# Performance work log

Measured on AMD Instinct MI355X. Metric: run time of the kernel, lower is better.

## Reference

```python
import jax, jax.numpy as jnp
import numpy as np

N = 8192
IN_F = 512
OUT_F = 256


def mish(x):
    return x * jnp.tanh(jax.nn.softplus(x))


def setup_inputs() -> dict:
    key = jax.random.key(0)
    k1, k2, k3, k4 = jax.random.split(key, 4)
    inp = jax.random.normal(k1, (N, IN_F), dtype=jnp.float32)
    # random binary adjacency mask (float, used via adj > 0), ensure self-loops
    adj = jax.random.randint(k2, (N, N), 0, 2).astype(jnp.float32)
    adj = adj.at[jnp.arange(N), jnp.arange(N)].set(1.0)
    # xavier_uniform_ init
    lim_W = float(np.sqrt(6.0 / (IN_F + OUT_F)))
    W = jax.random.uniform(k3, (IN_F, OUT_F), minval=-lim_W, maxval=lim_W, dtype=jnp.float32)
    lim_a = float(np.sqrt(6.0 / (2 * OUT_F + 1)))
    a = jax.random.uniform(k4, (2 * OUT_F, 1), minval=-lim_a, maxval=lim_a, dtype=jnp.float32)
    return {"input": inp, "adj": adj, "W": W, "a": a}


def reference(input, adj, W, a):
    # h: [N, F_out]
    h = input @ W
    f_out = W.shape[1]
    a1 = a[:f_out, 0]   # applied to source node (row i)
    a2 = a[f_out:, 0]   # applied to target node (col j)
    # e[i, j] = mish(h_i . a1 + h_j . a2)  -- identical math to the
    # O(N^2*2F) concat([h_i, h_j]) @ a in the torch reference.
    e = mish((h @ a1)[:, None] + (h @ a2)[None, :])  # [N, N]
    attention = jnp.where(adj > 0, e, jnp.float32(-9e15))
    attention = jax.nn.softmax(attention, axis=1)
    # dropout is inference-off (training=False)
    h_prime = attention @ h  # [N, F_out]
    return mish(h_prime)
```

## Files before the change

### kernel.cpp

```cpp
#include <hip/hip_runtime.h>

typedef __attribute__((ext_vector_type(8))) short short8;
typedef __attribute__((ext_vector_type(4))) float f32x4;

#define L2E 1.44269504088896340736f

__device__ __forceinline__ unsigned short f2bf(float x) {
    union { float f; unsigned int u; } v; v.f = x;
    unsigned int u = v.u;
    unsigned int r = (u + 0x7FFFu + ((u >> 16) & 1u)) >> 16;
    return (unsigned short)r;
}

__device__ __forceinline__ float mishf(float x) {
    float u = __builtin_amdgcn_exp2f(x * L2E);
    float t = u * (u + 2.0f);
    return x * t * __builtin_amdgcn_rcpf(t + 2.0f);
}

__device__ __forceinline__ short pw(unsigned int mb, int j, float sv, float s1v) {
    float xL = s1v + sv;
    float u = __builtin_amdgcn_exp2f(xL);
    float t = u * (u + 2.0f);
    float m = xL * t * __builtin_amdgcn_rcpf(t + 2.0f);
    float p = __builtin_amdgcn_exp2f(m);
    union { float f; unsigned int u; } b; b.f = p;
    unsigned short h = (unsigned short)((b.u + 0x8000u) >> 16);
    return ((mb >> j) & 1u) ? (short)h : (short)0;
}

typedef __attribute__((address_space(1))) const unsigned int guint;
typedef __attribute__((address_space(3))) unsigned int luint;
__device__ __forceinline__ void lds16(const void* g, void* l) {
    __builtin_amdgcn_global_load_lds((guint*)g, (luint*)l, 16, 0, 0);
}

__global__ __launch_bounds__(256) void k_pack(const float* __restrict__ adj,
                                              unsigned int* __restrict__ mask) {
    int wid = blockIdx.x * 4 + (threadIdx.x >> 6);
    int lane = threadIdx.x & 63;
    const float* row = adj + (size_t)wid * 8192 + lane;
    unsigned int* mrow = mask + wid * 256;
#pragma unroll 2
    for (int base = 0; base < 8192; base += 256) {
        float v0 = row[base];
        float v1 = row[base + 64];
        float v2 = row[base + 128];
        float v3 = row[base + 192];
        unsigned long long b0 = __ballot(v0 > 0.5f);
        unsigned long long b1 = __ballot(v1 > 0.5f);
        unsigned long long b2 = __ballot(v2 > 0.5f);
        unsigned long long b3 = __ballot(v3 > 0.5f);
        if (lane == 0) {
            *(ulonglong2*)(mrow + (base >> 5))     = make_ulonglong2(b0, b1);
            *(ulonglong2*)(mrow + (base >> 5) + 4) = make_ulonglong2(b2, b3);
        }
    }
}

__global__ void k_cvt_wt(const float* __restrict__ W, unsigned short* __restrict__ wt) {
    int c = blockIdx.x;
    int t = threadIdx.x;
    wt[c * 512 + t]       = f2bf(W[(size_t)t * 256 + c]);
    wt[c * 512 + t + 256] = f2bf(W[(size_t)(t + 256) * 256 + c]);
}

__global__ __launch_bounds__(256) void k_gemm_h(const float* __restrict__ input,
                                                const unsigned short* __restrict__ wt,
                                                const float* __restrict__ a,
                                                unsigned short* __restrict__ hbt,
                                                float* __restrict__ s1L,
                                                float* __restrict__ s2L) {
    __shared__ float red[2][4][16];
    int tid = threadIdx.x;
    int w = tid >> 6, lane = tid & 63, g = lane >> 4, r = lane & 15;
    int base = blockIdx.x * 16;

    f32x4 acc[4];
#pragma unroll
    for (int n = 0; n < 4; ++n) acc[n] = (f32x4)0.0f;

    const float* arow = input + (size_t)(base + r) * 512 + g * 8;
    const unsigned short* wp = wt + (size_t)(w * 64 + r) * 512 + g * 8;
#pragma unroll 4
    for (int kb = 0; kb < 512; kb += 32) {
        float4 a0 = *(const float4*)(arow + kb);
        float4 a1 = *(const float4*)(arow + kb + 4);
        short8 af;
        af[0] = (short)f2bf(a0.x); af[1] = (short)f2bf(a0.y);
        af[2] = (short)f2bf(a0.z); af[3] = (short)f2bf(a0.w);
        af[4] = (short)f2bf(a1.x); af[5] = (short)f2bf(a1.y);
        af[6] = (short)f2bf(a1.z); af[7] = (short)f2bf(a1.w);
#pragma unroll
        for (int n2 = 0; n2 < 4; ++n2) {
            short8 bf = *(const short8*)(wp + n2 * 8192 + kb);
            acc[n2] = __builtin_amdgcn_mfma_f32_16x16x32_bf16(af, bf, acc[n2], 0, 0, 0);
        }
    }
    int rowc = base + g * 4;
#pragma unroll
    for (int n2 = 0; n2 < 4; ++n2) {
        int col = w * 64 + n2 * 16 + r;
        ushort4 pk;
        pk.x = f2bf(acc[n2][0]); pk.y = f2bf(acc[n2][1]);
        pk.z = f2bf(acc[n2][2]); pk.w = f2bf(acc[n2][3]);
        *(ushort4*)(hbt + (size_t)col * 8192 + rowc) = pk;
    }
    float p1[4] = {0,0,0,0}, p2[4] = {0,0,0,0};
#pragma unroll
    for (int n2 = 0; n2 < 4; ++n2) {
        float a1v = a[w * 64 + n2 * 16 + r];
        float a2v = a[256 + w * 64 + n2 * 16 + r];
#pragma unroll
        for (int i = 0; i < 4; ++i) {
            p1[i] += acc[n2][i] * a1v;
            p2[i] += acc[n2][i] * a2v;
        }
    }
#pragma unroll
    for (int off = 8; off >= 1; off >>= 1) {
#pragma unroll
        for (int i = 0; i < 4; ++i) {
            p1[i] += __shfl_xor(p1[i], off);
            p2[i] += __shfl_xor(p2[i], off);
        }
    }
    if (r == 0) {
#pragma unroll
        for (int i = 0; i < 4; ++i) {
            red[0][w][g * 4 + i] = p1[i];
            red[1][w][g * 4 + i] = p2[i];
        }
    }
    __syncthreads();
    if (tid < 16) {
        float s1 = red[0][0][tid] + red[0][1][tid] + red[0][2][tid] + red[0][3][tid];
        float s2 = red[1][0][tid] + red[1][1][tid] + red[1][2][tid] + red[1][3][tid];
        s1L[base + tid] = s1 * L2E;
        s2L[base + tid] = s2 * L2E;
    }
}

__global__ __launch_bounds__(256, 2) void k_attn(const unsigned int* __restrict__ mask,
                                                 const unsigned short* __restrict__ hbt,
                                                 const float* __restrict__ s1L,
                                                 const float* __restrict__ s2L,
                                                 float* __restrict__ pS,
                                                 float* __restrict__ pZ) {
    __shared__ __align__(16) unsigned short tile[4][8192];

    int tid = threadIdx.x;
    int w = tid >> 6, lane = tid & 63, g = lane >> 4, r = lane & 15;
    int mb = blockIdx.x, chunk = blockIdx.y;
    int kc = chunk * 2048;
    int rowA = mb * 64 + w * 16 + r;
    float s1v = s1L[rowA];

    const unsigned int* mkp = mask + (size_t)rowA * 256 + chunk * 64;
    const float* svp = s2L + kc + g * 8;

    const unsigned short *hsrc0, *hsrc1, *hsrc2, *hsrc3;
    {
        int l2 = lane >> 2, sl = lane & 3;
        int r0 = 64 * w + l2,      ss0 = sl ^ ((r0 >> 1) & 3);
        int r1 = 64 * w + 16 + l2, ss1 = sl ^ ((r1 >> 1) & 3);
        int r2 = 64 * w + 32 + l2, ss2 = sl ^ ((r2 >> 1) & 3);
        int r3 = 64 * w + 48 + l2, ss3 = sl ^ ((r3 >> 1) & 3);
        hsrc0 = hbt + (size_t)r0 * 8192 + kc + ss0 * 8;
        hsrc1 = hbt + (size_t)r1 * 8192 + kc + ss1 * 8;
        hsrc2 = hbt + (size_t)r2 * 8192 + kc + ss2 * 8;
        hsrc3 = hbt + (size_t)r3 * 8192 + kc + ss3 * 8;
    }
    int sw = (r >> 1) & 3;
    int rdoff = r * 64 + ((g ^ sw) * 16);

    f32x4 acc[17];
#pragma unroll
    for (int n = 0; n < 17; ++n) acc[n] = (f32x4)0.0f;

    short8 onef;
    {
        short ov = (r == 0) ? (short)0x3F80 : (short)0;
#pragma unroll
        for (int j = 0; j < 8; ++j) onef[j] = ov;
    }

    unsigned int mkA, mkB, mkC, mkD;
    float4 svA0, svA1, svB0, svB1, svC0, svC1, svD0, svD1;

#define ISSUE(tt, bufn, MK, SV0, SV1) do {                                     \
        int t_ = (tt); if (t_ > 63) t_ = 63;                                   \
        int ko_ = t_ * 32;                                                     \
        char* lb_ = (char*)&tile[0][0] + (bufn) * 16384 + w * 4096;            \
        lds16(hsrc0 + ko_, lb_);                                               \
        lds16(hsrc1 + ko_, lb_ + 1024);                                        \
        lds16(hsrc2 + ko_, lb_ + 2048);                                        \
        lds16(hsrc3 + ko_, lb_ + 3072);                                        \
        MK = mkp[t_];                                                          \
        SV0 = *(const float4*)(svp + ko_);                                     \
        SV1 = *(const float4*)(svp + ko_ + 4);                                 \
    } while (0)

#define WAITBAR() do {                                                         \
        asm volatile("s_waitcnt vmcnt(7)" ::: "memory");                       \
        __builtin_amdgcn_sched_barrier(0);                                     \
        __builtin_amdgcn_s_barrier();                                          \
        __builtin_amdgcn_sched_barrier(0);                                     \
    } while (0)

#define COMPUTE(bufc, MK, SV0, SV1) do {                                       \
        unsigned int mby_ = (MK) >> (g * 8);                                   \
        short8 af_;                                                            \
        af_[0] = pw(mby_, 0, SV0.x, s1v);                                      \
        af_[1] = pw(mby_, 1, SV0.y, s1v);                                      \
        af_[2] = pw(mby_, 2, SV0.z, s1v);                                      \
        af_[3] = pw(mby_, 3, SV0.w, s1v);                                      \
        af_[4] = pw(mby_, 4, SV1.x, s1v);                                      \
        af_[5] = pw(mby_, 5, SV1.y, s1v);                                      \
        af_[6] = pw(mby_, 6, SV1.z, s1v);                                      \
        af_[7] = pw(mby_, 7, SV1.w, s1v);                                      \
        const char* tb_ = (const char*)&tile[0][0] + (bufc) * 16384 + rdoff;   \
        _Pragma("unroll")                                                      \
        for (int n_ = 0; n_ < 16; ++n_) {                                      \
            short8 bf_ = *(const short8*)(tb_ + n_ * 1024);                    \
            acc[n_] = __builtin_amdgcn_mfma_f32_16x16x32_bf16(af_, bf_, acc[n_], 0, 0, 0); \
        }                                                                      \
        acc[16] = __builtin_amdgcn_mfma_f32_16x16x32_bf16(af_, onef, acc[16], 0, 0, 0);    \
    } while (0)

    ISSUE(0, 0, mkA, svA0, svA1);
    ISSUE(1, 1, mkB, svB0, svB1);

    for (int s = 0; s < 64; s += 4) {
        WAITBAR();
        ISSUE(s + 2, 2, mkC, svC0, svC1);
        COMPUTE(0, mkA, svA0, svA1);
        WAITBAR();
        ISSUE(s + 3, 3, mkD, svD0, svD1);
        COMPUTE(1, mkB, svB0, svB1);
        WAITBAR();
        ISSUE(s + 4, 0, mkA, svA0, svA1);
        COMPUTE(2, mkC, svC0, svC1);
        WAITBAR();
        ISSUE(s + 5, 1, mkB, svB0, svB1);
        COMPUTE(3, mkD, svD0, svD1);
    }

    float* ps = pS + ((size_t)chunk << 21);
    int rowc = mb * 64 + w * 16 + g * 4;
#pragma unroll
    for (int n = 0; n < 16; ++n) {
#pragma unroll
        for (int i = 0; i < 4; ++i)
            ps[(size_t)(rowc + i) * 256 + n * 16 + r] = acc[n][i];
    }
    if (r == 0) {
        float* pz = pZ + chunk * 8192 + rowc;
#pragma unroll
        for (int i = 0; i < 4; ++i) pz[i] = acc[16][i];
    }
#undef ISSUE
#undef WAITBAR
#undef COMPUTE
}

__global__ void k_final(const float* __restrict__ pS, const float* __restrict__ pZ,
                        float* __restrict__ out) {
    int i = blockIdx.x;
    int f = threadIdx.x;
    size_t o = (size_t)i * 256 + f;
    float sv = pS[o] + pS[o + (1u << 21)] + pS[o + (2u << 21)] + pS[o + (3u << 21)];
    float z = pZ[i] + pZ[i + 8192] + pZ[i + 16384] + pZ[i + 24576];
    float hp = sv / z;
    out[o] = mishf(hp);
}

extern "C" void kernel_launch(void* const* d_in, const int* in_sizes, int n_in,
                              void* d_out, int out_size, void* d_ws, size_t ws_size,
                              hipStream_t stream) {
    const float* input = (const float*)d_in[0];
    const float* adj   = (const float*)d_in[1];
    const float* W     = (const float*)d_in[2];
    const float* a     = (const float*)d_in[3];
    float* out = (float*)d_out;

    char* ws = (char*)d_ws;
    unsigned short* wt   = (unsigned short*)ws;
    unsigned short* hbt  = (unsigned short*)(ws + 262144);
    float* s1L           = (float*)(ws + 4456448);
    float* s2L           = (float*)(ws + 4489216);
    unsigned int* mask   = (unsigned int*)(ws + 4521984);
    float* pS            = (float*)(ws + 12910592);
    float* pZ            = (float*)(ws + 46465024);

    hipLaunchKernelGGL(k_pack, dim3(2048), dim3(256), 0, stream, adj, mask);
    hipLaunchKernelGGL(k_cvt_wt, dim3(256), dim3(256), 0, stream, W, wt);
    hipLaunchKernelGGL(k_gemm_h, dim3(512), dim3(256), 0, stream, input, wt, a, hbt, s1L, s2L);
    hipLaunchKernelGGL(k_attn, dim3(128, 4), dim3(256), 0, stream, mask, hbt, s1L, s2L, pS, pZ);
    hipLaunchKernelGGL(k_final, dim3(8192), dim3(256), 0, stream, pS, pZ, out);
}
```

Baseline: 480.2 us.

## Restructure attention kernel to 32x32 MFMA tiles with factored exp and LDS-staged scores

Rewrites k_attn to use 512-thread blocks covering 128 rows, with 32x32x16 bf16 MFMAs and each wave pair splitting the feature dimension. This gives larger tiles and more reuse of each staged h tile. It factors exp2(s1+s2) as exp2(s1)*exp2(s2), with exp2(s2) precomputed in k_gemm_h, which removes one transcendental per attention element. The s2 and exp2(s2) vectors are staged once into LDS, and the pipeline becomes double-buffered 128-column stages with full vmcnt(0) barriers. The trade-offs are lower latency hiding from the full waits, higher LDS usage, only 256 blocks in the grid, and a possible overflow risk in the product e1*e2.

```diff
diff --git a/kernel.cpp b/kernel.cpp
--- a/kernel.cpp
+++ b/kernel.cpp
@@ -1,7 +1,8 @@
 #include <hip/hip_runtime.h>
 
-typedef __attribute__((ext_vector_type(8))) short short8;
-typedef __attribute__((ext_vector_type(4))) float f32x4;
+typedef __attribute__((ext_vector_type(8)))  short short8;
+typedef __attribute__((ext_vector_type(4)))  float f32x4;
+typedef __attribute__((ext_vector_type(16))) float f32x16;
 
 #define L2E 1.44269504088896340736f
 
@@ -18,21 +19,25 @@
     return x * t * __builtin_amdgcn_rcpf(t + 2.0f);
 }
 
-__device__ __forceinline__ short pw(unsigned int mb, int j, float sv, float s1v) {
-    float xL = s1v + sv;
-    float u = __builtin_amdgcn_exp2f(xL);
-    float t = u * (u + 2.0f);
-    float m = xL * t * __builtin_amdgcn_rcpf(t + 2.0f);
-    float p = __builtin_amdgcn_exp2f(m);
+__device__ __forceinline__ short pw2(unsigned int mby, int j, float svL, float ev,
+                                     float s1v, float e1v) {
+    float xL = s1v + svL;
+    float u  = e1v * ev;
+    float t  = u * (u + 2.0f);
+    float m  = xL * t * __builtin_amdgcn_rcpf(t + 2.0f);
+    float p  = __builtin_amdgcn_exp2f(m);
     union { float f; unsigned int u; } b; b.f = p;
     unsigned short h = (unsigned short)((b.u + 0x8000u) >> 16);
-    return ((mb >> j) & 1u) ? (short)h : (short)0;
+    return ((mby >> j) & 1u) ? (short)h : (short)0;
 }
 
 typedef __attribute__((address_space(1))) const unsigned int guint;
 typedef __attribute__((address_space(3))) unsigned int luint;
 __device__ __forceinline__ void lds16(const void* g, void* l) {
     __builtin_amdgcn_global_load_lds((guint*)g, (luint*)l, 16, 0, 0);
+}
+__device__ __forceinline__ void lds4(const void* g, void* l) {
+    __builtin_amdgcn_global_load_lds((guint*)g, (luint*)l, 4, 0, 0);
 }
 
 __global__ __launch_bounds__(256) void k_pack(const float* __restrict__ adj,
@@ -70,7 +75,8 @@
                                                 const float* __restrict__ a,
                                                 unsigned short* __restrict__ hbt,
                                                 float* __restrict__ s1L,
-                                                float* __restrict__ s2L) {
+                                                float* __restrict__ s2L,
+                                                float* __restrict__ e2g) {
     __shared__ float red[2][4][16];
     int tid = threadIdx.x;
     int w = tid >> 6, lane = tid & 63, g = lane >> 4, r = lane & 15;
@@ -137,130 +143,151 @@
         float s1 = red[0][0][tid] + red[0][1][tid] + red[0][2][tid] + red[0][3][tid];
         float s2 = red[1][0][tid] + red[1][1][tid] + red[1][2][tid] + red[1][3][tid];
         s1L[base + tid] = s1 * L2E;
-        s2L[base + tid] = s2 * L2E;
-    }
-}
-
-__global__ __launch_bounds__(256, 2) void k_attn(const unsigned int* __restrict__ mask,
+        float s2l = s2 * L2E;
+        s2L[base + tid] = s2l;
+        e2g[base + tid] = __builtin_amdgcn_exp2f(s2l);
+    }
+}
+
+__global__ __launch_bounds__(512, 2) void k_attn(const unsigned int* __restrict__ mask,
                                                  const unsigned short* __restrict__ hbt,
                                                  const float* __restrict__ s1L,
-                                                 const float* __restrict__ s2L,
+                                                 const float* __restrict__ s2Lg,
+                                                 const float* __restrict__ e2g,
                                                  float* __restrict__ pS,
                                                  float* __restrict__ pZ) {
-    __shared__ __align__(16) unsigned short tile[4][8192];
+    __shared__ __align__(16) unsigned short buf[2][32768];
+    __shared__ __align__(16) float s2s[2048];
+    __shared__ __align__(16) float e2s[2048];
 
     int tid = threadIdx.x;
-    int w = tid >> 6, lane = tid & 63, g = lane >> 4, r = lane & 15;
-    int mb = blockIdx.x, chunk = blockIdx.y;
+    int w = tid >> 6, lane = tid & 63;
+    int lo5 = lane & 31, hi = lane >> 5, lo7 = lane & 7;
+    int rg = w >> 1, fh = w & 1;
+    int bid = blockIdx.x;
+    int chunk = (bid & 7) >> 1;
+    int mb = ((bid >> 3) << 1) | (bid & 1);
     int kc = chunk * 2048;
-    int rowA = mb * 64 + w * 16 + r;
-    float s1v = s1L[rowA];
-
-    const unsigned int* mkp = mask + (size_t)rowA * 256 + chunk * 64;
-    const float* svp = s2L + kc + g * 8;
-
-    const unsigned short *hsrc0, *hsrc1, *hsrc2, *hsrc3;
+    int rowM = mb * 128 + rg * 32 + lo5;
+    float s1v = s1L[rowM];
+    float e1v = __builtin_amdgcn_exp2f(s1v);
+    const uint4* mk4 = (const uint4*)(mask + (size_t)rowM * 256 + (kc >> 5));
+
+    const unsigned short* hsrc = hbt + (size_t)(tid >> 4) * 8192 + kc
+                                     + (((tid & 15) ^ ((tid >> 4) & 7)) << 3);
     {
-        int l2 = lane >> 2, sl = lane & 3;
-        int r0 = 64 * w + l2,      ss0 = sl ^ ((r0 >> 1) & 3);
-        int r1 = 64 * w + 16 + l2, ss1 = sl ^ ((r1 >> 1) & 3);
-        int r2 = 64 * w + 32 + l2, ss2 = sl ^ ((r2 >> 1) & 3);
-        int r3 = 64 * w + 48 + l2, ss3 = sl ^ ((r3 >> 1) & 3);
-        hsrc0 = hbt + (size_t)r0 * 8192 + kc + ss0 * 8;
-        hsrc1 = hbt + (size_t)r1 * 8192 + kc + ss1 * 8;
-        hsrc2 = hbt + (size_t)r2 * 8192 + kc + ss2 * 8;
-        hsrc3 = hbt + (size_t)r3 * 8192 + kc + ss3 * 8;
-    }
-    int sw = (r >> 1) & 3;
-    int rdoff = r * 64 + ((g ^ sw) * 16);
-
-    f32x4 acc[17];
-#pragma unroll
-    for (int n = 0; n < 17; ++n) acc[n] = (f32x4)0.0f;
+        const float* s2src = s2Lg + kc + tid;
+        const float* e2src = e2g  + kc + tid;
+#pragma unroll
+        for (int q = 0; q < 4; ++q) {
+            lds4(s2src + q * 512, &s2s[q * 512 + tid]);
+            lds4(e2src + q * 512, &e2s[q * 512 + tid]);
+        }
+    }
+
+    int fb = fh * 32768 + lo5 * 256;
+
+    f32x16 acc[4];
+#pragma unroll
+    for (int n = 0; n < 4; ++n) acc[n] = (f32x16)0.0f;
+    f32x16 accz = (f32x16)0.0f;
 
     short8 onef;
     {
-        short ov = (r == 0) ? (short)0x3F80 : (short)0;
+        short ov = (lo5 == 0) ? (short)0x3F80 : (short)0;
 #pragma unroll
         for (int j = 0; j < 8; ++j) onef[j] = ov;
     }
 
-    unsigned int mkA, mkB, mkC, mkD;
-    float4 svA0, svA1, svB0, svB1, svC0, svC1, svD0, svD1;
-
-#define ISSUE(tt, bufn, MK, SV0, SV1) do {                                     \
-        int t_ = (tt); if (t_ > 63) t_ = 63;                                   \
-        int ko_ = t_ * 32;                                                     \
-        char* lb_ = (char*)&tile[0][0] + (bufn) * 16384 + w * 4096;            \
-        lds16(hsrc0 + ko_, lb_);                                               \
-        lds16(hsrc1 + ko_, lb_ + 1024);                                        \
-        lds16(hsrc2 + ko_, lb_ + 2048);                                        \
-        lds16(hsrc3 + ko_, lb_ + 3072);                                        \
-        MK = mkp[t_];                                                          \
-        SV0 = *(const float4*)(svp + ko_);                                     \
-        SV1 = *(const float4*)(svp + ko_ + 4);                                 \
+#define STAGE(ss, p) do {                                                      \
+        int kb_ = (ss) * 128;                                                  \
+        _Pragma("unroll")                                                      \
+        for (int j_ = 0; j_ < 8; ++j_)                                         \
+            lds16(hsrc + (size_t)j_ * 262144 + kb_,                            \
+                  (char*)&buf[p][0] + j_ * 8192 + tid * 16);                   \
     } while (0)
 
-#define WAITBAR() do {                                                         \
-        asm volatile("s_waitcnt vmcnt(7)" ::: "memory");                       \
+#define VBAR() do {                                                            \
+        asm volatile("s_waitcnt vmcnt(0)" ::: "memory");                       \
         __builtin_amdgcn_sched_barrier(0);                                     \
         __builtin_amdgcn_s_barrier();                                          \
         __builtin_amdgcn_sched_barrier(0);                                     \
     } while (0)
 
-#define COMPUTE(bufc, MK, SV0, SV1) do {                                       \
-        unsigned int mby_ = (MK) >> (g * 8);                                   \
-        short8 af_;                                                            \
-        af_[0] = pw(mby_, 0, SV0.x, s1v);                                      \
-        af_[1] = pw(mby_, 1, SV0.y, s1v);                                      \
-        af_[2] = pw(mby_, 2, SV0.z, s1v);                                      \
-        af_[3] = pw(mby_, 3, SV0.w, s1v);                                      \
-        af_[4] = pw(mby_, 4, SV1.x, s1v);                                      \
-        af_[5] = pw(mby_, 5, SV1.y, s1v);                                      \
-        af_[6] = pw(mby_, 6, SV1.z, s1v);                                      \
-        af_[7] = pw(mby_, 7, SV1.w, s1v);                                      \
-        const char* tb_ = (const char*)&tile[0][0] + (bufc) * 16384 + rdoff;   \
+#define COMPUTE(p, MK, ss) do {                                                \
+        const char* tb_ = (const char*)&buf[p][0] + fb;                        \
         _Pragma("unroll")                                                      \
-        for (int n_ = 0; n_ < 16; ++n_) {                                      \
-            short8 bf_ = *(const short8*)(tb_ + n_ * 1024);                    \
-            acc[n_] = __builtin_amdgcn_mfma_f32_16x16x32_bf16(af_, bf_, acc[n_], 0, 0, 0); \
+        for (int ks = 0; ks < 8; ++ks) {                                       \
+            unsigned int wbits = ((ks >> 1) == 0) ? (MK).x :                   \
+                                 ((ks >> 1) == 1) ? (MK).y :                   \
+                                 ((ks >> 1) == 2) ? (MK).z : (MK).w;           \
+            unsigned int mby = (wbits >> (((ks & 1) << 4) + (hi << 3))) & 0xffu;\
+            int cb_ = (ss) * 128 + ks * 16 + hi * 8;                           \
+            float4 sv0 = *(const float4*)&s2s[cb_];                            \
+            float4 sv1 = *(const float4*)&s2s[cb_ + 4];                        \
+            float4 ev0 = *(const float4*)&e2s[cb_];                            \
+            float4 ev1 = *(const float4*)&e2s[cb_ + 4];                        \
+            short8 af;                                                         \
+            af[0] = pw2(mby, 0, sv0.x, ev0.x, s1v, e1v);                       \
+            af[1] = pw2(mby, 1, sv0.y, ev0.y, s1v, e1v);                       \
+            af[2] = pw2(mby, 2, sv0.z, ev0.z, s1v, e1v);                       \
+            af[3] = pw2(mby, 3, sv0.w, ev0.w, s1v, e1v);                       \
+            af[4] = pw2(mby, 4, sv1.x, ev1.x, s1v, e1v);                       \
+            af[5] = pw2(mby, 5, sv1.y, ev1.y, s1v, e1v);                       \
+            af[6] = pw2(mby, 6, sv1.z, ev1.z, s1v, e1v);                       \
+            af[7] = pw2(mby, 7, sv1.w, ev1.w, s1v, e1v);                       \
+            const char* tbb_ = tb_ + ((((ks * 2 + hi) ^ lo7)) << 4);           \
+            short8 b0 = *(const short8*)(tbb_);                                \
+            short8 b1 = *(const short8*)(tbb_ + 8192);                         \
+            short8 b2 = *(const short8*)(tbb_ + 16384);                       \
+            short8 b3 = *(const short8*)(tbb_ + 24576);                       \
+            acc[0] = __builtin_amdgcn_mfma_f32_32x32x16_bf16(af, b0, acc[0], 0, 0, 0); \
+            acc[1] = __builtin_amdgcn_mfma_f32_32x32x16_bf16(af, b1, acc[1], 0, 0, 0); \
+            acc[2] = __builtin_amdgcn_mfma_f32_32x32x16_bf16(af, b2, acc[2], 0, 0, 0); \
+            acc[3] = __builtin_amdgcn_mfma_f32_32x32x16_bf16(af, b3, acc[3], 0, 0, 0); \
+            accz   = __builtin_amdgcn_mfma_f32_32x32x16_bf16(af, onef, accz, 0, 0, 0); \
         }                                                                      \
-        acc[16] = __builtin_amdgcn_mfma_f32_16x16x32_bf16(af_, onef, acc[16], 0, 0, 0);    \
     } while (0)
 
-    ISSUE(0, 0, mkA, svA0, svA1);
-    ISSUE(1, 1, mkB, svB0, svB1);
-
-    for (int s = 0; s < 64; s += 4) {
-        WAITBAR();
-        ISSUE(s + 2, 2, mkC, svC0, svC1);
-        COMPUTE(0, mkA, svA0, svA1);
-        WAITBAR();
-        ISSUE(s + 3, 3, mkD, svD0, svD1);
-        COMPUTE(1, mkB, svB0, svB1);
-        WAITBAR();
-        ISSUE(s + 4, 0, mkA, svA0, svA1);
-        COMPUTE(2, mkC, svC0, svC1);
-        WAITBAR();
-        ISSUE(s + 5, 1, mkB, svB0, svB1);
-        COMPUTE(3, mkD, svD0, svD1);
-    }
-
-    float* ps = pS + ((size_t)chunk << 21);
-    int rowc = mb * 64 + w * 16 + g * 4;
-#pragma unroll
-    for (int n = 0; n < 16; ++n) {
-#pragma unroll
-        for (int i = 0; i < 4; ++i)
-            ps[(size_t)(rowc + i) * 256 + n * 16 + r] = acc[n][i];
-    }
-    if (r == 0) {
-        float* pz = pZ + chunk * 8192 + rowc;
-#pragma unroll
-        for (int i = 0; i < 4; ++i) pz[i] = acc[16][i];
-    }
-#undef ISSUE
-#undef WAITBAR
+    STAGE(0, 0);
+    uint4 mkA = mk4[0];
+    uint4 mkB;
+    VBAR();
+
+    for (int ss = 0; ss < 16; ss += 2) {
+        mkB = mk4[ss + 1];
+        STAGE(ss + 1, 1);
+        COMPUTE(0, mkA, ss);
+        VBAR();
+        int nx = (ss + 2 < 16) ? (ss + 2) : 15;
+        mkA = mk4[nx];
+        STAGE(nx, 0);
+        COMPUTE(1, mkB, ss + 1);
+        VBAR();
+    }
+
+    {
+        float* ps = pS + ((size_t)chunk << 21)
+                  + (size_t)(mb * 128 + rg * 32 + hi * 4) * 256 + fh * 128 + lo5;
+#pragma unroll
+        for (int n = 0; n < 4; ++n) {
+#pragma unroll
+            for (int e = 0; e < 16; ++e) {
+                int rl = (e & 3) + ((e >> 2) << 3);
+                ps[(size_t)rl * 256 + n * 32] = acc[n][e];
+            }
+        }
+    }
+    if (fh == 0 && lo5 == 0) {
+        float* pz = pZ + chunk * 8192 + mb * 128 + rg * 32 + hi * 4;
+#pragma unroll
+        for (int e = 0; e < 16; ++e) {
+            int rl = (e & 3) + ((e >> 2) << 3);
+            pz[rl] = accz[e];
+        }
+    }
+#undef STAGE
+#undef VBAR
 #undef COMPUTE
 }
 
@@ -289,13 +316,14 @@
     unsigned short* hbt  = (unsigned short*)(ws + 262144);
     float* s1L           = (float*)(ws + 4456448);
     float* s2L           = (float*)(ws + 4489216);
-    unsigned int* mask   = (unsigned int*)(ws + 4521984);
-    float* pS            = (float*)(ws + 12910592);
-    float* pZ            = (float*)(ws + 46465024);
+    float* e2g           = (float*)(ws + 4521984);
+    unsigned int* mask   = (unsigned int*)(ws + 4554752);
+    float* pS            = (float*)(ws + 12943360);
+    float* pZ            = (float*)(ws + 46497792);
 
     hipLaunchKernelGGL(k_pack, dim3(2048), dim3(256), 0, stream, adj, mask);
     hipLaunchKernelGGL(k_cvt_wt, dim3(256), dim3(256), 0, stream, W, wt);
-    hipLaunchKernelGGL(k_gemm_h, dim3(512), dim3(256), 0, stream, input, wt, a, hbt, s1L, s2L);
-    hipLaunchKernelGGL(k_attn, dim3(128, 4), dim3(256), 0, stream, mask, hbt, s1L, s2L, pS, pZ);
+    hipLaunchKernelGGL(k_gemm_h, dim3(512), dim3(256), 0, stream, input, wt, a, hbt, s1L, s2L, e2g);
+    hipLaunchKernelGGL(k_attn, dim3(256), dim3(512), 0, stream, mask, hbt, s1L, s2L, e2g, pS, pZ);
     hipLaunchKernelGGL(k_final, dim3(8192), dim3(256), 0, stream, pS, pZ, out);
 }
```

New measurement: 496.5 us. +3.4%, slower.

## Rewrite attention kernel with 32x32 MFMA tiles and 8-way key split

Applied to the files above, without the earlier changes.

Replaces the 16x16x32 MFMA attention kernel with one using 32x32x16 bf16 MFMA. Each block now covers 128 query rows and each wave 32 rows. The key dimension is split into 8 chunks instead of 4, and the s2 logits are staged once into LDS rather than loaded per step. The larger tiles are meant to raise reuse of the h tile per LDS read and cut per-element instruction overhead, while the extra chunks keep the grid at 512 blocks. In exchange, the partial-sum buffer and the final reduction double in size.

```diff
diff --git a/kernel.cpp b/kernel.cpp
--- a/kernel.cpp
+++ b/kernel.cpp
@@ -1,7 +1,8 @@
 #include <hip/hip_runtime.h>
 
-typedef __attribute__((ext_vector_type(8))) short short8;
-typedef __attribute__((ext_vector_type(4))) float f32x4;
+typedef __attribute__((ext_vector_type(8)))  short short8;
+typedef __attribute__((ext_vector_type(4)))  float f32x4;
+typedef __attribute__((ext_vector_type(16))) float f32x16;
 
 #define L2E 1.44269504088896340736f
 
@@ -18,15 +19,9 @@
     return x * t * __builtin_amdgcn_rcpf(t + 2.0f);
 }
 
-__device__ __forceinline__ short pw(unsigned int mb, int j, float sv, float s1v) {
-    float xL = s1v + sv;
-    float u = __builtin_amdgcn_exp2f(xL);
-    float t = u * (u + 2.0f);
-    float m = xL * t * __builtin_amdgcn_rcpf(t + 2.0f);
-    float p = __builtin_amdgcn_exp2f(m);
+__device__ __forceinline__ short bfr(float p) {
     union { float f; unsigned int u; } b; b.f = p;
-    unsigned short h = (unsigned short)((b.u + 0x8000u) >> 16);
-    return ((mb >> j) & 1u) ? (short)h : (short)0;
+    return (short)((b.u + 0x8000u) >> 16);
 }
 
 typedef __attribute__((address_space(1))) const unsigned int guint;
@@ -141,127 +136,133 @@
     }
 }
 
-__global__ __launch_bounds__(256, 2) void k_attn(const unsigned int* __restrict__ mask,
-                                                 const unsigned short* __restrict__ hbt,
-                                                 const float* __restrict__ s1L,
-                                                 const float* __restrict__ s2L,
-                                                 float* __restrict__ pS,
-                                                 float* __restrict__ pZ) {
-    __shared__ __align__(16) unsigned short tile[4][8192];
+__global__ __launch_bounds__(256, 2) void k_pv(const unsigned int* __restrict__ mask,
+                                               const unsigned short* __restrict__ hbt,
+                                               const float* __restrict__ s1Lg,
+                                               const float* __restrict__ s2Lg,
+                                               float* __restrict__ pS,
+                                               float* __restrict__ pZ) {
+    __shared__ __align__(16) unsigned short buf[4][8192];
+    __shared__ __align__(16) float s2s[1024];
 
     int tid = threadIdx.x;
-    int w = tid >> 6, lane = tid & 63, g = lane >> 4, r = lane & 15;
+    int w = tid >> 6, lane = tid & 63;
+    int lo5 = lane & 31, hi = lane >> 5;
     int mb = blockIdx.x, chunk = blockIdx.y;
-    int kc = chunk * 2048;
-    int rowA = mb * 64 + w * 16 + r;
-    float s1v = s1L[rowA];
-
-    const unsigned int* mkp = mask + (size_t)rowA * 256 + chunk * 64;
-    const float* svp = s2L + kc + g * 8;
-
-    const unsigned short *hsrc0, *hsrc1, *hsrc2, *hsrc3;
-    {
-        int l2 = lane >> 2, sl = lane & 3;
-        int r0 = 64 * w + l2,      ss0 = sl ^ ((r0 >> 1) & 3);
-        int r1 = 64 * w + 16 + l2, ss1 = sl ^ ((r1 >> 1) & 3);
-        int r2 = 64 * w + 32 + l2, ss2 = sl ^ ((r2 >> 1) & 3);
-        int r3 = 64 * w + 48 + l2, ss3 = sl ^ ((r3 >> 1) & 3);
-        hsrc0 = hbt + (size_t)r0 * 8192 + kc + ss0 * 8;
-        hsrc1 = hbt + (size_t)r1 * 8192 + kc + ss1 * 8;
-        hsrc2 = hbt + (size_t)r2 * 8192 + kc + ss2 * 8;
-        hsrc3 = hbt + (size_t)r3 * 8192 + kc + ss3 * 8;
-    }
-    int sw = (r >> 1) & 3;
-    int rdoff = r * 64 + ((g ^ sw) * 16);
-
-    f32x4 acc[17];
-#pragma unroll
-    for (int n = 0; n < 17; ++n) acc[n] = (f32x4)0.0f;
+    int kc = chunk * 1024;
+    int rowbase = mb * 128 + w * 32;
+    float s1v = s1Lg[rowbase + lo5];
+    const unsigned int* mkp = mask + (size_t)(rowbase + lo5) * 256 + chunk * 32;
+
+    int feat0 = tid >> 2;
+    const unsigned short* hsrc = hbt + (size_t)feat0 * 8192 + kc
+                                     + (((tid & 3) ^ ((feat0 >> 1) & 3)) << 3);
+    int rdswz = (lo5 >> 1) & 3;
+
+    f32x16 acc[8];
+#pragma unroll
+    for (int n = 0; n < 8; ++n) acc[n] = (f32x16)0.0f;
+    f32x16 accz = (f32x16)0.0f;
 
     short8 onef;
     {
-        short ov = (r == 0) ? (short)0x3F80 : (short)0;
+        short ov = (lo5 == 0) ? (short)0x3F80 : (short)0;
 #pragma unroll
         for (int j = 0; j < 8; ++j) onef[j] = ov;
     }
 
-    unsigned int mkA, mkB, mkC, mkD;
-    float4 svA0, svA1, svB0, svB1, svC0, svC1, svD0, svD1;
-
-#define ISSUE(tt, bufn, MK, SV0, SV1) do {                                     \
-        int t_ = (tt); if (t_ > 63) t_ = 63;                                   \
-        int ko_ = t_ * 32;                                                     \
-        char* lb_ = (char*)&tile[0][0] + (bufn) * 16384 + w * 4096;            \
-        lds16(hsrc0 + ko_, lb_);                                               \
-        lds16(hsrc1 + ko_, lb_ + 1024);                                        \
-        lds16(hsrc2 + ko_, lb_ + 2048);                                        \
-        lds16(hsrc3 + ko_, lb_ + 3072);                                        \
-        MK = mkp[t_];                                                          \
-        SV0 = *(const float4*)(svp + ko_);                                     \
-        SV1 = *(const float4*)(svp + ko_ + 4);                                 \
+    unsigned int mk0, mk1, mk2, mk3;
+
+#define STAGE(ss, p) do {                                                      \
+        int ko_ = (((ss) < 32) ? (ss) : 31) * 32;                              \
+        char* lb_ = (char*)&buf[0][0] + (p) * 16384 + tid * 16;                \
+        _Pragma("unroll")                                                      \
+        for (int j_ = 0; j_ < 4; ++j_)                                         \
+            lds16(hsrc + (size_t)j_ * 524288 + ko_, lb_ + j_ * 4096);          \
     } while (0)
 
-#define WAITBAR() do {                                                         \
-        asm volatile("s_waitcnt vmcnt(7)" ::: "memory");                       \
+#define BAR() do {                                                             \
         __builtin_amdgcn_sched_barrier(0);                                     \
         __builtin_amdgcn_s_barrier();                                          \
         __builtin_amdgcn_sched_barrier(0);                                     \
     } while (0)
 
-#define COMPUTE(bufc, MK, SV0, SV1) do {                                       \
-        unsigned int mby_ = (MK) >> (g * 8);                                   \
-        short8 af_;                                                            \
-        af_[0] = pw(mby_, 0, SV0.x, s1v);                                      \
-        af_[1] = pw(mby_, 1, SV0.y, s1v);                                      \
-        af_[2] = pw(mby_, 2, SV0.z, s1v);                                      \
-        af_[3] = pw(mby_, 3, SV0.w, s1v);                                      \
-        af_[4] = pw(mby_, 4, SV1.x, s1v);                                      \
-        af_[5] = pw(mby_, 5, SV1.y, s1v);                                      \
-        af_[6] = pw(mby_, 6, SV1.z, s1v);                                      \
-        af_[7] = pw(mby_, 7, SV1.w, s1v);                                      \
-        const char* tb_ = (const char*)&tile[0][0] + (bufc) * 16384 + rdoff;   \
+#define VW() do {                                                              \
+        asm volatile("s_waitcnt vmcnt(10)" ::: "memory");                      \
+        __builtin_amdgcn_sched_barrier(0);                                     \
+    } while (0)
+
+#define COMP(p, MK, ss) do {                                                   \
+        const char* tb_ = (const char*)&buf[0][0] + (p) * 16384 + lo5 * 64;    \
         _Pragma("unroll")                                                      \
-        for (int n_ = 0; n_ < 16; ++n_) {                                      \
-            short8 bf_ = *(const short8*)(tb_ + n_ * 1024);                    \
-            acc[n_] = __builtin_amdgcn_mfma_f32_16x16x32_bf16(af_, bf_, acc[n_], 0, 0, 0); \
+        for (int ksub = 0; ksub < 2; ++ksub) {                                 \
+            int svb_ = (ss) * 128 + ksub * 64 + hi * 32;                       \
+            f32x4 sv0 = *(const f32x4*)((const char*)s2s + svb_);              \
+            f32x4 sv1 = *(const f32x4*)((const char*)s2s + svb_ + 16);         \
+            int sh_ = ksub * 16 + hi * 8;                                      \
+            short8 af;                                                         \
+            _Pragma("unroll")                                                  \
+            for (int j_ = 0; j_ < 8; ++j_) {                                   \
+                float svL = (j_ < 4) ? sv0[j_ & 3] : sv1[j_ & 3];              \
+                float xL = s1v + svL;                                          \
+                float u = __builtin_amdgcn_exp2f(xL);                          \
+                float t = u * (u + 2.0f);                                      \
+                float m = xL * t * __builtin_amdgcn_rcpf(t + 2.0f);            \
+                float pv = __builtin_amdgcn_exp2f(m);                          \
+                pv = ((MK >> (sh_ + j_)) & 1u) ? pv : 0.0f;                    \
+                af[j_] = bfr(pv);                                              \
+            }                                                                  \
+            const char* tbl_ = tb_ + ((((ksub * 2 + hi) ^ rdswz)) << 4);       \
+            _Pragma("unroll")                                                  \
+            for (int n_ = 0; n_ < 8; ++n_) {                                   \
+                short8 bf_ = *(const short8*)(tbl_ + n_ * 2048);               \
+                acc[n_] = __builtin_amdgcn_mfma_f32_32x32x16_bf16(af, bf_, acc[n_], 0, 0, 0); \
+            }                                                                  \
+            accz = __builtin_amdgcn_mfma_f32_32x32x16_bf16(af, onef, accz, 0, 0, 0);          \
         }                                                                      \
-        acc[16] = __builtin_amdgcn_mfma_f32_16x16x32_bf16(af_, onef, acc[16], 0, 0, 0);    \
     } while (0)
 
-    ISSUE(0, 0, mkA, svA0, svA1);
-    ISSUE(1, 1, mkB, svB0, svB1);
-
-    for (int s = 0; s < 64; s += 4) {
-        WAITBAR();
-        ISSUE(s + 2, 2, mkC, svC0, svC1);
-        COMPUTE(0, mkA, svA0, svA1);
-        WAITBAR();
-        ISSUE(s + 3, 3, mkD, svD0, svD1);
-        COMPUTE(1, mkB, svB0, svB1);
-        WAITBAR();
-        ISSUE(s + 4, 0, mkA, svA0, svA1);
-        COMPUTE(2, mkC, svC0, svC1);
-        WAITBAR();
-        ISSUE(s + 5, 1, mkB, svB0, svB1);
-        COMPUTE(3, mkD, svD0, svD1);
-    }
-
-    float* ps = pS + ((size_t)chunk << 21);
-    int rowc = mb * 64 + w * 16 + g * 4;
-#pragma unroll
-    for (int n = 0; n < 16; ++n) {
-#pragma unroll
-        for (int i = 0; i < 4; ++i)
-            ps[(size_t)(rowc + i) * 256 + n * 16 + r] = acc[n][i];
-    }
-    if (r == 0) {
-        float* pz = pZ + chunk * 8192 + rowc;
-#pragma unroll
-        for (int i = 0; i < 4; ++i) pz[i] = acc[16][i];
-    }
-#undef ISSUE
-#undef WAITBAR
-#undef COMPUTE
+    lds16(s2Lg + kc + tid * 4, (char*)s2s + tid * 16);
+    STAGE(0, 0); mk0 = mkp[0];
+    STAGE(1, 1); mk1 = mkp[1];
+    asm volatile("s_waitcnt vmcnt(10)" ::: "memory");
+    __builtin_amdgcn_sched_barrier(0);
+    __builtin_amdgcn_s_barrier();
+
+    for (int s = 0; s < 32; s += 4) {
+        BAR(); STAGE(s + 2, 2); mk2 = mkp[(s + 2 < 32) ? s + 2 : 31];
+        VW();  COMP(0, mk0, s);
+        BAR(); STAGE(s + 3, 3); mk3 = mkp[(s + 3 < 32) ? s + 3 : 31];
+        VW();  COMP(1, mk1, s + 1);
+        BAR(); STAGE(s + 4, 0); mk0 = mkp[(s + 4 < 32) ? s + 4 : 31];
+        VW();  COMP(2, mk2, s + 2);
+        BAR(); STAGE(s + 5, 1); mk1 = mkp[(s + 5 < 32) ? s + 5 : 31];
+        VW();  COMP(3, mk3, s + 3);
+    }
+
+    {
+        float* ps = pS + ((size_t)chunk << 21) + (size_t)rowbase * 256;
+#pragma unroll
+        for (int n = 0; n < 8; ++n) {
+#pragma unroll
+            for (int e = 0; e < 16; ++e) {
+                int rl = (e & 3) + ((e >> 2) << 3) + hi * 4;
+                ps[(size_t)rl * 256 + n * 32 + lo5] = acc[n][e];
+            }
+        }
+    }
+    if (lo5 == 0) {
+        float* pz = pZ + chunk * 8192 + rowbase;
+#pragma unroll
+        for (int e = 0; e < 16; ++e) {
+            int rl = (e & 3) + ((e >> 2) << 3) + hi * 4;
+            pz[rl] = accz[e];
+        }
+    }
+#undef STAGE
+#undef BAR
+#undef VW
+#undef COMP
 }
 
 __global__ void k_final(const float* __restrict__ pS, const float* __restrict__ pZ,
@@ -269,10 +270,13 @@
     int i = blockIdx.x;
     int f = threadIdx.x;
     size_t o = (size_t)i * 256 + f;
-    float sv = pS[o] + pS[o + (1u << 21)] + pS[o + (2u << 21)] + pS[o + (3u << 21)];
-    float z = pZ[i] + pZ[i + 8192] + pZ[i + 16384] + pZ[i + 24576];
-    float hp = sv / z;
-    out[o] = mishf(hp);
+    float sv = 0.0f, z = 0.0f;
+#pragma unroll
+    for (int c = 0; c < 8; ++c) {
+        sv += pS[o + ((size_t)c << 21)];
+        z  += pZ[c * 8192 + i];
+    }
+    out[o] = mishf(sv / z);
 }
 
 extern "C" void kernel_launch(void* const* d_in, const int* in_sizes, int n_in,
@@ -291,11 +295,11 @@
     float* s2L           = (float*)(ws + 4489216);
     unsigned int* mask   = (unsigned int*)(ws + 4521984);
     float* pS            = (float*)(ws + 12910592);
-    float* pZ            = (float*)(ws + 46465024);
+    float* pZ            = (float*)(ws + 80019456);
 
     hipLaunchKernelGGL(k_pack, dim3(2048), dim3(256), 0, stream, adj, mask);
     hipLaunchKernelGGL(k_cvt_wt, dim3(256), dim3(256), 0, stream, W, wt);
     hipLaunchKernelGGL(k_gemm_h, dim3(512), dim3(256), 0, stream, input, wt, a, hbt, s1L, s2L);
-    hipLaunchKernelGGL(k_attn, dim3(128, 4), dim3(256), 0, stream, mask, hbt, s1L, s2L, pS, pZ);
+    hipLaunchKernelGGL(k_pv, dim3(64, 8), dim3(256), 0, stream, mask, hbt, s1L, s2L, pS, pZ);
     hipLaunchKernelGGL(k_final, dim3(8192), dim3(256), 0, stream, pS, pZ, out);
 }
```

Measured after the change: 478.2 us. About the same (-0.4%).
